# Kernel tuning notes

Measured on AMD Instinct MI355X. Metric: run time of the kernel, lower is better.

Reference implementation:

```python
import jax, jax.numpy as jnp
import numpy as np

L, B, T, H = 3, 128, 256, 512  # layers, batch, seq_max_len, n_hidden


def setup_inputs() -> dict:
    key = jax.random.key(0)
    k0, k1, k2 = jax.random.split(key, 3)
    scale = 1.0 / np.sqrt(H).astype(np.float32)
    x = jax.random.normal(k0, (B, T, H), jnp.float32)
    kernels = jax.random.normal(k1, (L, H, 3 * H), jnp.float32) * scale
    rec_kernels = jax.random.normal(k2, (L, H, 3 * H), jnp.float32) * scale
    biases = jnp.zeros((L, 2, 3 * H), jnp.float32)  # [input_bias, recurrent_bias] (reset_after=True)
    return {"x": x, "kernels": kernels, "rec_kernels": rec_kernels, "biases": biases}


def _gru_layer(x, h0, Wk, Wu, b):
    # x: [B,T,D], h0: [B,H], Wk: [D,3H], Wu: [H,3H], b: [2,3H]
    # Keras GRU, reset_after=True, gate order (z, r, h)
    xp = jnp.einsum('btd,dh->bth', x, Wk) + b[0]  # precompute input projections
    br = b[1]

    def step(h, xp_t):
        rec = h @ Wu + br                      # [B,3H]
        xz, xr, xh = jnp.split(xp_t, 3, axis=-1)
        rz, rr, rh = jnp.split(rec, 3, axis=-1)
        z = jax.nn.sigmoid(xz + rz)
        r = jax.nn.sigmoid(xr + rr)
        hh = jnp.tanh(xh + r * rh)
        h_new = z * h + (1.0 - z) * hh
        return h_new, h_new

    last_h, seq = jax.lax.scan(step, h0, jnp.swapaxes(xp, 0, 1))  # seq: [T,B,H]
    return jnp.swapaxes(seq, 0, 1), last_h


def reference(x, kernels, rec_kernels, biases):
    Bc, Tc, _ = x.shape
    Hd = kernels.shape[2] // 3
    state = None
    for l in range(kernels.shape[0]):
        # layer l>0 receives previous layer's final state as initial_state
        h0 = jnp.zeros((Bc, Hd), x.dtype) if state is None else state
        x, state = _gru_layer(x, h0, kernels[l], rec_kernels[l], biases[l])
    # tf.reshape(states, (-1, H)) then tf.split(seq_max_len, axis=0) -> stack == reshape to [T, B, H]
    states_h = x.reshape(-1, Hd).reshape(Tc, -1, Hd)
    return states_h, state
```

## Files before the change

kernel.cpp:

```cpp
#include <hip/hip_runtime.h>
#include <hip/hip_bf16.h>

#define NL  3
#define NB  128
#define NT  256
#define NH  512
#define NH3 1536
#define NBH (NB*NH)
#define NM  (NB*NT)

typedef __bf16 bf16x8 __attribute__((ext_vector_type(8)));
typedef unsigned short u16x8 __attribute__((ext_vector_type(8)));
typedef float  floatx4 __attribute__((ext_vector_type(4)));
typedef __hip_bfloat16 bf16;

__device__ __forceinline__ floatx4 mfma16(bf16x8 a, bf16x8 b, floatx4 c) {
  return __builtin_amdgcn_mfma_f32_16x16x32_bf16(a, b, c, 0, 0, 0);
}
__device__ __forceinline__ void gload16(const void* g, void* l) {
  __builtin_amdgcn_global_load_lds(
      (const __attribute__((address_space(1))) unsigned int*)g,
      (__attribute__((address_space(3))) unsigned int*)l, 16, 0, 0);
}
__device__ __forceinline__ float fsig(float x)  { return 1.0f / (1.0f + __expf(-x)); }
__device__ __forceinline__ float ftanh(float x) { return 2.0f / (1.0f + __expf(-2.0f*x)) - 1.0f; }
__device__ __forceinline__ float b2f(unsigned short u) {
  unsigned v = (unsigned)u << 16; float f; __builtin_memcpy(&f, &v, 4); return f;
}
__device__ __forceinline__ unsigned short f2b(float f) {
  bf16 h = __float2bfloat16(f); unsigned short u; __builtin_memcpy(&u, &h, 2); return u;
}

__global__ void transpose_cvt_kernel(const float* __restrict__ in, bf16* __restrict__ out) {
  __shared__ float tile[32][33];
  int l = blockIdx.z;
  int n0 = blockIdx.x * 32, k0 = blockIdx.y * 32;
  const float* src = in + (size_t)l * NH * NH3;
  bf16* dst = out + (size_t)l * NH3 * NH;
  int tx = threadIdx.x, ty = threadIdx.y;
#pragma unroll
  for (int i = 0; i < 4; i++)
    tile[ty + 8*i][tx] = src[(size_t)(k0 + ty + 8*i) * NH3 + n0 + tx];
  __syncthreads();
#pragma unroll
  for (int i = 0; i < 4; i++)
    dst[(size_t)(n0 + ty + 8*i) * NH + k0 + tx] = __float2bfloat16(tile[tx][ty + 8*i]);
}

__global__ void cvt_x_kernel(const float* __restrict__ in, bf16* __restrict__ out) {
  size_t i = (size_t)blockIdx.x * blockDim.x + threadIdx.x;
  float4 v = ((const float4*)in)[i];
  ushort4 pk;
  pk.x = f2b(v.x); pk.y = f2b(v.y); pk.z = f2b(v.z); pk.w = f2b(v.w);
  ((ushort4*)out)[i] = pk;
}

__global__ void __launch_bounds__(256, 2) gemm_xp_kernel(
    const bf16* __restrict__ A, const bf16* __restrict__ Bt,
    const float* __restrict__ bias, bf16* __restrict__ C, int a_mode)
{
  __shared__ char alds[16384];
  __shared__ char blds[16384];
  int tid = threadIdx.x;
  int lane = tid & 63, w = tid >> 6;
  int mblk = blockIdx.x, nblk = blockIdx.y;
  int wm = w >> 1, wn = w & 1;
  int klane = (lane >> 4) * 8;
  int r0 = 2*w*16 + (lane & 15);
  size_t arow0, arow1;
  if (a_mode == 0) {
    arow0 = ((size_t)r0 * NT + mblk) * NH;
    arow1 = ((size_t)(r0 + 16) * NT + mblk) * NH;
  } else {
    arow0 = (size_t)(mblk*128 + r0) * NH;
    arow1 = arow0 + (size_t)16 * NH;
  }
  size_t brow0 = (size_t)(nblk*128 + 2*w*16 + (lane & 15)) * NH;
  size_t brow1 = brow0 + (size_t)16 * NH;

  floatx4 acc[4][4];
#pragma unroll
  for (int i = 0; i < 4; i++)
#pragma unroll
    for (int j = 0; j < 4; j++) acc[i][j] = (floatx4){0.f, 0.f, 0.f, 0.f};

  for (int kk = 0; kk < 8; kk++) {
    int kb = kk*64 + klane;
#pragma unroll
    for (int kt = 0; kt < 2; kt++) {
      int kg = kb + kt*32;
      gload16(A  + arow0 + kg, alds + (kt*8 + 2*w    ) * 1024);
      gload16(A  + arow1 + kg, alds + (kt*8 + 2*w + 1) * 1024);
      gload16(Bt + brow0 + kg, blds + (kt*8 + 2*w    ) * 1024);
      gload16(Bt + brow1 + kg, blds + (kt*8 + 2*w + 1) * 1024);
    }
    __syncthreads();
#pragma unroll
    for (int kt = 0; kt < 2; kt++) {
      bf16x8 af[4], bfr[4];
#pragma unroll
      for (int i = 0; i < 4; i++) af[i]  = *(const bf16x8*)(alds + ((kt*8 + wm*4 + i)*64 + lane)*16);
#pragma unroll
      for (int j = 0; j < 4; j++) bfr[j] = *(const bf16x8*)(blds + ((kt*8 + wn*4 + j)*64 + lane)*16);
#pragma unroll
      for (int i = 0; i < 4; i++)
#pragma unroll
        for (int j = 0; j < 4; j++)
          acc[i][j] = mfma16(af[i], bfr[j], acc[i][j]);
    }
    __syncthreads();
  }
  int cl = lane & 15, rbase = (lane >> 4) * 4;
#pragma unroll
  for (int i = 0; i < 4; i++) {
    int gm = mblk*128 + wm*64 + i*16 + rbase;
#pragma unroll
    for (int j = 0; j < 4; j++) {
      int gn = nblk*128 + wn*64 + j*16 + cl;
      float bv = bias[gn];
#pragma unroll
      for (int r = 0; r < 4; r++)
        C[(size_t)(gm + r) * NH3 + gn] = __float2bfloat16(acc[i][j][r] + bv);
    }
  }
}

__global__ void __launch_bounds__(256, 1) gru_scan_kernel(
    const bf16*  __restrict__ wuT,
    const float* __restrict__ br,
    const bf16*  __restrict__ xp,
    const bf16*  __restrict__ h0bf,
    bf16*        __restrict__ seq,
    const float* __restrict__ hf0,
    float*       __restrict__ outBTH,
    float*       __restrict__ hfinal,
    unsigned*    __restrict__ cnt, unsigned tgtbase)
{
  __shared__ bf16  h_raw[16 * 520];
  __shared__ float rec_l[16 * 388];
  __shared__ int   deadflag;
  int tid = threadIdx.x, lane = tid & 63, w = tid >> 6;
  int g = blockIdx.x >> 2, c = blockIdx.x & 3;
  int bb0 = g * 16;
  int klane = (lane >> 4) * 8;
  if (tid == 0) deadflag = 0;

  bf16x8 wf[6][16];
  float  brv[6];
#pragma unroll
  for (int i = 0; i < 6; i++) {
    int lc = w*96 + i*16 + (lane & 15);
    int ng = (lc >> 7) * NH + c*128 + (lc & 127);
    brv[i] = br[ng];
    const bf16* wrow = wuT + (size_t)ng * NH + klane;
#pragma unroll
    for (int kt = 0; kt < 16; kt++) wf[i][kt] = *(const bf16x8*)(wrow + kt*32);
  }

  int row = tid >> 4, jj = (tid & 15) * 8;
  int bb = bb0 + row, hc0 = c*128 + jj;
  float hreg[8];
#pragma unroll
  for (int q = 0; q < 8; q++)
    hreg[q] = hf0 ? hf0[(size_t)bb * NH + hc0 + q] : 0.0f;

  int chunk = tid & 15;
  bf16* lds_st = h_raw + row*520 + chunk*32;
  const char* abase = (const char*)h_raw + (lane & 15)*1040 + (lane >> 4)*16;
  float* rrow = rec_l + row*388;

  for (int t = 0; t < NT; t++) {
    const bf16* xrow = xp + ((size_t)t*NB + bb)*NH3 + c*128 + jj;
    u16x8 xz8 = *(const u16x8*)(xrow);
    u16x8 xr8 = *(const u16x8*)(xrow + 512);
    u16x8 xh8 = *(const u16x8*)(xrow + 1024);

    if (t > 0) {
      if (tid == 0) {
        unsigned tgt = tgtbase + 4u * (unsigned)t;
        long sp = 0;
        while (__hip_atomic_load(cnt + g, __ATOMIC_RELAXED, __HIP_MEMORY_SCOPE_AGENT) < tgt) {
          __builtin_amdgcn_s_sleep(1);
          if (++sp > (1L << 20)) { deadflag = 1; break; }
        }
      }
      __syncthreads();
      if (deadflag) return;
    }

    {
      const bf16* hs = (t == 0) ? h0bf : (seq + (size_t)t * NBH);
      if (hs == nullptr) {
#pragma unroll
        for (int j2 = 0; j2 < 8; j2++) *(unsigned long long*)(lds_st + j2*4) = 0ull;
      } else {
        const unsigned long long* gs =
            (const unsigned long long*)(hs + (size_t)bb * NH + chunk*32);
#pragma unroll
        for (int j2 = 0; j2 < 8; j2++)
          *(unsigned long long*)(lds_st + j2*4) =
              __hip_atomic_load(gs + j2, __ATOMIC_RELAXED, __HIP_MEMORY_SCOPE_AGENT);
      }
    }
    __syncthreads();

    floatx4 acc[6];
#pragma unroll
    for (int i = 0; i < 6; i++) acc[i] = (floatx4){0.f, 0.f, 0.f, 0.f};
#pragma unroll
    for (int kt = 0; kt < 16; kt++) {
      bf16x8 ha = *(const bf16x8*)(abase + kt*64);
#pragma unroll
      for (int i = 0; i < 6; i++) acc[i] = mfma16(ha, wf[i][kt], acc[i]);
    }
    {
      int ccol = lane & 15, rb = (lane >> 4) * 4;
#pragma unroll
      for (int i = 0; i < 6; i++) {
        int lc0 = w*96 + i*16;
#pragma unroll
        for (int r = 0; r < 4; r++)
          rec_l[(rb + r)*388 + lc0 + ccol] = acc[i][r] + brv[i];
      }
    }
    __syncthreads();

    {
      float4 rz0 = *(float4*)(rrow + jj),       rz1 = *(float4*)(rrow + jj + 4);
      float4 rr0 = *(float4*)(rrow + 128 + jj), rr1 = *(float4*)(rrow + 128 + jj + 4);
      float4 rh0 = *(float4*)(rrow + 256 + jj), rh1 = *(float4*)(rrow + 256 + jj + 4);
      float rz[8] = {rz0.x,rz0.y,rz0.z,rz0.w, rz1.x,rz1.y,rz1.z,rz1.w};
      float rr[8] = {rr0.x,rr0.y,rr0.z,rr0.w, rr1.x,rr1.y,rr1.z,rr1.w};
      float rh[8] = {rh0.x,rh0.y,rh0.z,rh0.w, rh1.x,rh1.y,rh1.z,rh1.w};
      unsigned short pk[8];
#pragma unroll
      for (int q = 0; q < 8; q++) {
        float z  = fsig(b2f(xz8[q]) + rz[q]);
        float r  = fsig(b2f(xr8[q]) + rr[q]);
        float hh = ftanh(b2f(xh8[q]) + r * rh[q]);
        float hn = z * hreg[q] + (1.0f - z) * hh;
        hreg[q] = hn;
        pk[q] = f2b(hn);
      }
      bf16* so = seq + (size_t)(t+1) * NBH + (size_t)bb * NH + hc0;
      unsigned long long p0, p1;
      __builtin_memcpy(&p0, &pk[0], 8); __builtin_memcpy(&p1, &pk[4], 8);
      __hip_atomic_store((unsigned long long*)so,     p0, __ATOMIC_RELAXED, __HIP_MEMORY_SCOPE_AGENT);
      __hip_atomic_store((unsigned long long*)so + 1, p1, __ATOMIC_RELAXED, __HIP_MEMORY_SCOPE_AGENT);
      if (outBTH) {
        float* o = outBTH + ((size_t)bb * NT + t) * NH + hc0;
        *(float4*)o       = (float4){hreg[0], hreg[1], hreg[2], hreg[3]};
        *(float4*)(o + 4) = (float4){hreg[4], hreg[5], hreg[6], hreg[7]};
      }
      if (t == NT-1) {
        float* o = hfinal + (size_t)bb * NH + hc0;
        *(float4*)o       = (float4){hreg[0], hreg[1], hreg[2], hreg[3]};
        *(float4*)(o + 4) = (float4){hreg[4], hreg[5], hreg[6], hreg[7]};
      }
    }

    if (t < NT-1) {
      __syncthreads();
      if (tid == 0)
        __hip_atomic_fetch_add(cnt + g, 1u, __ATOMIC_RELAXED, __HIP_MEMORY_SCOPE_AGENT);
    }
  }
}

extern "C" void kernel_launch(void* const* d_in, const int* in_sizes, int n_in,
                              void* d_out, int out_size, void* d_ws, size_t ws_size,
                              hipStream_t stream) {
  const float* x   = (const float*)d_in[0];
  const float* wk  = (const float*)d_in[1];
  const float* wu  = (const float*)d_in[2];
  const float* bis = (const float*)d_in[3];
  float* out = (float*)d_out;

  const size_t REQ = 144048192;
  if (ws_size < REQ) {
    hipMemsetAsync(d_out, 0, (size_t)out_size * 4, stream);
    return;
  }
  char* ws = (char*)d_ws;
  bf16*  wkT   = (bf16*)(ws);
  bf16*  wuT   = (bf16*)(ws + 4718592);
  bf16*  xp    = (bf16*)(ws + 9437184);
  bf16*  seq   = (bf16*)(ws + 110100480);
  bf16*  xb    = seq;
  float* hlast = (float*)(ws + 143785984);
  unsigned* cnt = (unsigned*)(ws + 144048128);

  hipMemsetAsync(cnt, 0, 64, stream);
  transpose_cvt_kernel<<<dim3(48,16,3), dim3(32,8), 0, stream>>>(wk, wkT);
  transpose_cvt_kernel<<<dim3(48,16,3), dim3(32,8), 0, stream>>>(wu, wuT);
  cvt_x_kernel<<<(NM*NH/4)/256, 256, 0, stream>>>(x, xb);

  const size_t WS = (size_t)NH3 * NH;

  gemm_xp_kernel<<<dim3(256,12), 256, 0, stream>>>(xb, wkT, bis + 0*2*NH3, xp, 0);
  gru_scan_kernel<<<32, 256, 0, stream>>>(wuT, bis + 0*2*NH3 + NH3, xp,
      nullptr, seq, nullptr, nullptr, hlast, cnt, 0u);
  gemm_xp_kernel<<<dim3(256,12), 256, 0, stream>>>(seq + NBH, wkT + WS, bis + 1*2*NH3, xp, 1);
  gru_scan_kernel<<<32, 256, 0, stream>>>(wuT + WS, bis + 1*2*NH3 + NH3, xp,
      seq + (size_t)NT * NBH, seq, hlast, nullptr, hlast, cnt, 1020u);
  gemm_xp_kernel<<<dim3(256,12), 256, 0, stream>>>(seq + NBH, wkT + 2*WS, bis + 2*2*NH3, xp, 1);
  gru_scan_kernel<<<32, 256, 0, stream>>>(wuT + 2*WS, bis + 2*2*NH3 + NH3, xp,
      seq + (size_t)NT * NBH, seq, hlast, out, out + (size_t)NT * NBH, cnt, 2040u);

  (void)in_sizes; (void)n_in; (void)out_size; (void)ws_size;
}
```

Measured before the change: 4.130 ms.

## Restructure GRU scan with 8 waves and swapped MFMA operands to drop LDS gate round-trip

The recurrent scan kernel now uses 512 threads per block, so each wave holds weights for only 16 hidden columns across the three gates (48 fragments instead of 96). The MFMA operands are swapped so each lane's accumulator already holds the z, r and h gate values for its own outputs. This removes the LDS staging buffer for recurrent results and one barrier per timestep. The hidden state is written into LDS in an MFMA-friendly swizzled layout. The change lowers register pressure and per-step synchronisation, at the cost of more waves contending on each step's barrier and spin-wait. The kernel interface is also simplified with a layer index, and the deadlock timeout is lengthened.

```diff
diff --git a/kernel.cpp b/kernel.cpp
--- a/kernel.cpp
+++ b/kernel.cpp
@@ -10,9 +10,9 @@
 #define NM  (NB*NT)
 
 typedef __bf16 bf16x8 __attribute__((ext_vector_type(8)));
-typedef unsigned short u16x8 __attribute__((ext_vector_type(8)));
 typedef float  floatx4 __attribute__((ext_vector_type(4)));
 typedef __hip_bfloat16 bf16;
+typedef unsigned long long u64;
 
 __device__ __forceinline__ floatx4 mfma16(bf16x8 a, bf16x8 b, floatx4 c) {
   return __builtin_amdgcn_mfma_f32_16x16x32_bf16(a, b, c, 0, 0, 0);
@@ -29,6 +29,12 @@
 }
 __device__ __forceinline__ unsigned short f2b(float f) {
   bf16 h = __float2bfloat16(f); unsigned short u; __builtin_memcpy(&u, &h, 2); return u;
+}
+__device__ __forceinline__ u64 ald(const u64* p) {
+  return __hip_atomic_load(p, __ATOMIC_RELAXED, __HIP_MEMORY_SCOPE_AGENT);
+}
+__device__ __forceinline__ void ast(u64* p, u64 v) {
+  __hip_atomic_store(p, v, __ATOMIC_RELAXED, __HIP_MEMORY_SCOPE_AGENT);
 }
 
 __global__ void transpose_cvt_kernel(const float* __restrict__ in, bf16* __restrict__ out) {
@@ -125,55 +131,50 @@
   }
 }
 
-__global__ void __launch_bounds__(256, 1) gru_scan_kernel(
+__global__ void __launch_bounds__(512, 2) gru_scan_kernel(
     const bf16*  __restrict__ wuT,
     const float* __restrict__ br,
     const bf16*  __restrict__ xp,
-    const bf16*  __restrict__ h0bf,
     bf16*        __restrict__ seq,
-    const float* __restrict__ hf0,
-    float*       __restrict__ outBTH,
-    float*       __restrict__ hfinal,
-    unsigned*    __restrict__ cnt, unsigned tgtbase)
+    float*       __restrict__ hlast,
+    float*       __restrict__ out,
+    unsigned*    __restrict__ cnt,
+    unsigned tgtbase, int layer)
 {
-  __shared__ bf16  h_raw[16 * 520];
-  __shared__ float rec_l[16 * 388];
-  __shared__ int   deadflag;
+  __shared__ __align__(16) char h_raw[16384];
+  __shared__ int deadflag;
   int tid = threadIdx.x, lane = tid & 63, w = tid >> 6;
   int g = blockIdx.x >> 2, c = blockIdx.x & 3;
   int bb0 = g * 16;
-  int klane = (lane >> 4) * 8;
+  int r16 = lane & 15, h4 = lane >> 4;
+  int srow = tid & 15, ssc = tid >> 4;
   if (tid == 0) deadflag = 0;
 
-  bf16x8 wf[6][16];
-  float  brv[6];
-#pragma unroll
-  for (int i = 0; i < 6; i++) {
-    int lc = w*96 + i*16 + (lane & 15);
-    int ng = (lc >> 7) * NH + c*128 + (lc & 127);
-    brv[i] = br[ng];
-    const bf16* wrow = wuT + (size_t)ng * NH + klane;
-#pragma unroll
-    for (int kt = 0; kt < 16; kt++) wf[i][kt] = *(const bf16x8*)(wrow + kt*32);
-  }
-
-  int row = tid >> 4, jj = (tid & 15) * 8;
-  int bb = bb0 + row, hc0 = c*128 + jj;
-  float hreg[8];
-#pragma unroll
-  for (int q = 0; q < 8; q++)
-    hreg[q] = hf0 ? hf0[(size_t)bb * NH + hc0 + q] : 0.0f;
-
-  int chunk = tid & 15;
-  bf16* lds_st = h_raw + row*520 + chunk*32;
-  const char* abase = (const char*)h_raw + (lane & 15)*1040 + (lane >> 4)*16;
-  float* rrow = rec_l + row*388;
+  bf16x8 wf[3][16];
+  float  bv[3][4];
+#pragma unroll
+  for (int G = 0; G < 3; G++) {
+    const bf16* wrow = wuT + ((size_t)(G*NH + c*128 + w*16 + r16)) * NH + h4*8;
+#pragma unroll
+    for (int kt = 0; kt < 16; kt++) wf[G][kt] = *(const bf16x8*)(wrow + kt*32);
+#pragma unroll
+    for (int q = 0; q < 4; q++) bv[G][q] = br[G*NH + c*128 + w*16 + h4*4 + q];
+  }
+
+  float hreg[4];
+  if (layer == 0) {
+    hreg[0] = hreg[1] = hreg[2] = hreg[3] = 0.0f;
+  } else {
+    const float* hsrc = hlast + (size_t)(bb0 + r16) * NH + c*128 + w*16 + h4*4;
+    float4 v = *(const float4*)hsrc;
+    hreg[0] = v.x; hreg[1] = v.y; hreg[2] = v.z; hreg[3] = v.w;
+  }
+
+  u64* seqU = (u64*)seq;
 
   for (int t = 0; t < NT; t++) {
-    const bf16* xrow = xp + ((size_t)t*NB + bb)*NH3 + c*128 + jj;
-    u16x8 xz8 = *(const u16x8*)(xrow);
-    u16x8 xr8 = *(const u16x8*)(xrow + 512);
-    u16x8 xh8 = *(const u16x8*)(xrow + 1024);
+    const u64* xq = (const u64*)(xp + ((size_t)t*NB + bb0 + r16)*NH3 + c*128 + w*16 + h4*4);
+    u64 xv0 = xq[0], xv1 = xq[128], xv2 = xq[256];
 
     if (t > 0) {
       if (tid == 0) {
@@ -181,89 +182,72 @@
         long sp = 0;
         while (__hip_atomic_load(cnt + g, __ATOMIC_RELAXED, __HIP_MEMORY_SCOPE_AGENT) < tgt) {
           __builtin_amdgcn_s_sleep(1);
-          if (++sp > (1L << 20)) { deadflag = 1; break; }
+          if (++sp > (1L << 22)) { deadflag = 1; break; }
         }
       }
       __syncthreads();
       if (deadflag) return;
     }
 
-    {
-      const bf16* hs = (t == 0) ? h0bf : (seq + (size_t)t * NBH);
-      if (hs == nullptr) {
-#pragma unroll
-        for (int j2 = 0; j2 < 8; j2++) *(unsigned long long*)(lds_st + j2*4) = 0ull;
-      } else {
-        const unsigned long long* gs =
-            (const unsigned long long*)(hs + (size_t)bb * NH + chunk*32);
-#pragma unroll
-        for (int j2 = 0; j2 < 8; j2++)
-          *(unsigned long long*)(lds_st + j2*4) =
-              __hip_atomic_load(gs + j2, __ATOMIC_RELAXED, __HIP_MEMORY_SCOPE_AGENT);
+    if (layer == 0 && t == 0) {
+      *(int4*)(h_raw + tid*32)      = (int4){0,0,0,0};
+      *(int4*)(h_raw + tid*32 + 16) = (int4){0,0,0,0};
+    } else {
+      int slot = (t == 0) ? NT : t;
+      const u64* src = seqU + ((size_t)slot*NBH + (size_t)(bb0 + srow)*NH) / 4;
+#pragma unroll
+      for (int d = 0; d < 2; d++) {
+        int sc = ssc + d*32;
+        u64 q0 = ald(src + sc*2), q1 = ald(src + sc*2 + 1);
+        u64* dst = (u64*)(h_raw + (((sc >> 2)*64) + (sc & 3)*16 + srow)*16);
+        dst[0] = q0; dst[1] = q1;
       }
     }
     __syncthreads();
 
-    floatx4 acc[6];
-#pragma unroll
-    for (int i = 0; i < 6; i++) acc[i] = (floatx4){0.f, 0.f, 0.f, 0.f};
+    floatx4 ac0 = (floatx4){0,0,0,0}, ac1 = (floatx4){0,0,0,0}, ac2 = (floatx4){0,0,0,0};
 #pragma unroll
     for (int kt = 0; kt < 16; kt++) {
-      bf16x8 ha = *(const bf16x8*)(abase + kt*64);
-#pragma unroll
-      for (int i = 0; i < 6; i++) acc[i] = mfma16(ha, wf[i][kt], acc[i]);
-    }
-    {
-      int ccol = lane & 15, rb = (lane >> 4) * 4;
-#pragma unroll
-      for (int i = 0; i < 6; i++) {
-        int lc0 = w*96 + i*16;
-#pragma unroll
-        for (int r = 0; r < 4; r++)
-          rec_l[(rb + r)*388 + lc0 + ccol] = acc[i][r] + brv[i];
+      bf16x8 hb = *(const bf16x8*)(h_raw + (kt*64 + lane)*16);
+      ac0 = mfma16(wf[0][kt], hb, ac0);
+      ac1 = mfma16(wf[1][kt], hb, ac1);
+      ac2 = mfma16(wf[2][kt], hb, ac2);
+    }
+
+    unsigned short pk[4];
+#pragma unroll
+    for (int q = 0; q < 4; q++) {
+      float rz = ac0[q] + bv[0][q];
+      float rr = ac1[q] + bv[1][q];
+      float rh = ac2[q] + bv[2][q];
+      float xz = b2f((unsigned short)(xv0 >> (16*q)));
+      float xr = b2f((unsigned short)(xv1 >> (16*q)));
+      float xh = b2f((unsigned short)(xv2 >> (16*q)));
+      float z  = fsig(xz + rz);
+      float r  = fsig(xr + rr);
+      float hh = ftanh(xh + r * rh);
+      float hn = z * hreg[q] + (1.0f - z) * hh;
+      hreg[q] = hn;
+      pk[q] = f2b(hn);
+    }
+    u64 pv; __builtin_memcpy(&pv, pk, 8);
+    ast(seqU + ((size_t)(t+1)*NBH + (size_t)(bb0 + r16)*NH)/4 + c*32 + w*4 + h4, pv);
+
+    if (layer == 2) {
+      float* o = out + ((size_t)(bb0 + r16)*NT + t)*NH + c*128 + w*16 + h4*4;
+      *(float4*)o = (float4){hreg[0], hreg[1], hreg[2], hreg[3]};
+      if (t == NT - 1) {
+        float* o2 = out + (size_t)NM*NH + (size_t)(bb0 + r16)*NH + c*128 + w*16 + h4*4;
+        *(float4*)o2 = (float4){hreg[0], hreg[1], hreg[2], hreg[3]};
       }
-    }
-    __syncthreads();
-
-    {
-      float4 rz0 = *(float4*)(rrow + jj),       rz1 = *(float4*)(rrow + jj + 4);
-      float4 rr0 = *(float4*)(rrow + 128 + jj), rr1 = *(float4*)(rrow + 128 + jj + 4);
-      float4 rh0 = *(float4*)(rrow + 256 + jj), rh1 = *(float4*)(rrow + 256 + jj + 4);
-      float rz[8] = {rz0.x,rz0.y,rz0.z,rz0.w, rz1.x,rz1.y,rz1.z,rz1.w};
-      float rr[8] = {rr0.x,rr0.y,rr0.z,rr0.w, rr1.x,rr1.y,rr1.z,rr1.w};
-      float rh[8] = {rh0.x,rh0.y,rh0.z,rh0.w, rh1.x,rh1.y,rh1.z,rh1.w};
-      unsigned short pk[8];
-#pragma unroll
-      for (int q = 0; q < 8; q++) {
-        float z  = fsig(b2f(xz8[q]) + rz[q]);
-        float r  = fsig(b2f(xr8[q]) + rr[q]);
-        float hh = ftanh(b2f(xh8[q]) + r * rh[q]);
-        float hn = z * hreg[q] + (1.0f - z) * hh;
-        hreg[q] = hn;
-        pk[q] = f2b(hn);
-      }
-      bf16* so = seq + (size_t)(t+1) * NBH + (size_t)bb * NH + hc0;
-      unsigned long long p0, p1;
-      __builtin_memcpy(&p0, &pk[0], 8); __builtin_memcpy(&p1, &pk[4], 8);
-      __hip_atomic_store((unsigned long long*)so,     p0, __ATOMIC_RELAXED, __HIP_MEMORY_SCOPE_AGENT);
-      __hip_atomic_store((unsigned long long*)so + 1, p1, __ATOMIC_RELAXED, __HIP_MEMORY_SCOPE_AGENT);
-      if (outBTH) {
-        float* o = outBTH + ((size_t)bb * NT + t) * NH + hc0;
-        *(float4*)o       = (float4){hreg[0], hreg[1], hreg[2], hreg[3]};
-        *(float4*)(o + 4) = (float4){hreg[4], hreg[5], hreg[6], hreg[7]};
-      }
-      if (t == NT-1) {
-        float* o = hfinal + (size_t)bb * NH + hc0;
-        *(float4*)o       = (float4){hreg[0], hreg[1], hreg[2], hreg[3]};
-        *(float4*)(o + 4) = (float4){hreg[4], hreg[5], hreg[6], hreg[7]};
-      }
-    }
-
-    if (t < NT-1) {
-      __syncthreads();
-      if (tid == 0)
-        __hip_atomic_fetch_add(cnt + g, 1u, __ATOMIC_RELAXED, __HIP_MEMORY_SCOPE_AGENT);
-    }
+    } else if (t == NT - 1) {
+      float* o = hlast + (size_t)(bb0 + r16)*NH + c*128 + w*16 + h4*4;
+      *(float4*)o = (float4){hreg[0], hreg[1], hreg[2], hreg[3]};
+    }
+
+    __syncthreads();
+    if (tid == 0 && t < NT - 1)
+      __hip_atomic_fetch_add(cnt + g, 1u, __ATOMIC_RELAXED, __HIP_MEMORY_SCOPE_AGENT);
   }
 }
 
@@ -298,14 +282,14 @@
   const size_t WS = (size_t)NH3 * NH;
 
   gemm_xp_kernel<<<dim3(256,12), 256, 0, stream>>>(xb, wkT, bis + 0*2*NH3, xp, 0);
-  gru_scan_kernel<<<32, 256, 0, stream>>>(wuT, bis + 0*2*NH3 + NH3, xp,
-      nullptr, seq, nullptr, nullptr, hlast, cnt, 0u);
+  gru_scan_kernel<<<32, 512, 0, stream>>>(wuT, bis + 0*2*NH3 + NH3, xp,
+      seq, hlast, nullptr, cnt, 0u, 0);
   gemm_xp_kernel<<<dim3(256,12), 256, 0, stream>>>(seq + NBH, wkT + WS, bis + 1*2*NH3, xp, 1);
-  gru_scan_kernel<<<32, 256, 0, stream>>>(wuT + WS, bis + 1*2*NH3 + NH3, xp,
-      seq + (size_t)NT * NBH, seq, hlast, nullptr, hlast, cnt, 1020u);
+  gru_scan_kernel<<<32, 512, 0, stream>>>(wuT + WS, bis + 1*2*NH3 + NH3, xp,
+      seq, hlast, nullptr, cnt, 1020u, 1);
   gemm_xp_kernel<<<dim3(256,12), 256, 0, stream>>>(seq + NBH, wkT + 2*WS, bis + 2*2*NH3, xp, 1);
-  gru_scan_kernel<<<32, 256, 0, stream>>>(wuT + 2*WS, bis + 2*2*NH3 + NH3, xp,
-      seq + (size_t)NT * NBH, seq, hlast, out, out + (size_t)NT * NBH, cnt, 2040u);
+  gru_scan_kernel<<<32, 512, 0, stream>>>(wuT + 2*WS, bis + 2*2*NH3 + NH3, xp,
+      seq, hlast, out, cnt, 2040u, 2);
 
   (void)in_sizes; (void)n_in; (void)out_size; (void)ws_size;
 }
```

After: 3.499 ms. 15.3% less time.
